# Kernel tuning notes

Hardware: AMD Instinct MI355X
Metric: run time of the kernel (lower is better)

## Reference

```python
import jax, jax.numpy as jnp
import numpy as np

B = 512
DIM_X = 128
DIM_Y = 128
HIDDEN = 512


def setup_inputs() -> dict:
    key = jax.random.key(0)
    kx, ky, kw1, kw2 = jax.random.split(key, 4)
    x = jax.random.normal(kx, (B, DIM_X), dtype=jnp.float32)
    y = jax.random.normal(ky, (B, DIM_Y), dtype=jnp.float32)
    # Glorot-ish scaling for the Dense layers
    W1 = jax.random.normal(kw1, (DIM_X + DIM_Y, HIDDEN), dtype=jnp.float32) * (1.0 / np.sqrt(DIM_X + DIM_Y))
    b1 = jnp.zeros((HIDDEN,), dtype=jnp.float32)
    W2 = jax.random.normal(kw2, (HIDDEN, 1), dtype=jnp.float32) * (1.0 / np.sqrt(HIDDEN))
    b2 = jnp.zeros((1,), dtype=jnp.float32)
    return {"x": x, "y": y, "W1": W1, "b1": b1, "W2": W2, "b2": b2}


def reference(x, y, W1, b1, W2, b2):
    # scores[i, j] = f(concat(x_i, y_j)) with f = Dense(512, relu) -> Dense(1).
    # Since the first Dense is linear in the concatenated input, split W1 into
    # the x-block and y-block and broadcast-sum instead of materializing the
    # [B*B, dim_x+dim_y] concat tensor (same math as tile+concat+matmul).
    dim_x = x.shape[1]
    hx = x @ W1[:dim_x]          # [B, H]
    hy = y @ W1[dim_x:]          # [B, H]
    h = jax.nn.relu(hx[:, None, :] + hy[None, :, :] + b1)  # [B, B, H]
    scores = jnp.einsum('ijh,h->ij', h, W2[:, 0]) + b2[0]   # [B, B]
    return scores
```

## Files before the change

### kernel.cpp

```cpp
#include <hip/hip_runtime.h>


#define BATCH 512
#define DX    128
#define HID   512

typedef _Float16 half2_t __attribute__((ext_vector_type(2)));

static __device__ __forceinline__ half2_t u2h(unsigned int u) {
    union { unsigned int u; half2_t h; } c; c.u = u; return c.h;
}
static __device__ __forceinline__ unsigned int h2u(half2_t h) {
    union { half2_t h; unsigned int u; } c; c.h = h; return c.u;
}

__global__ __launch_bounds__(256) void proj_kernel(
    const float* __restrict__ x, const float* __restrict__ y,
    const float* __restrict__ W1, const float* __restrict__ b1,
    _Float16* __restrict__ hxy)
{
    const int part = blockIdx.y;
    const int row0 = blockIdx.x * 8;
    const int h    = blockIdx.z * 256 + threadIdx.x;
    const float* __restrict__ src = part ? y : x;
    const float* __restrict__ W   = W1 + part * DX * HID;

    __shared__ float s[8][DX];
    {
        const int t = threadIdx.x;
        const int r = t >> 5, c4 = (t & 31) << 2;
        const float4 v = *(const float4*)&src[(row0 + r) * DX + c4];
        s[r][c4] = v.x; s[r][c4 + 1] = v.y; s[r][c4 + 2] = v.z; s[r][c4 + 3] = v.w;
    }
    __syncthreads();

    float acc[8] = {0.f, 0.f, 0.f, 0.f, 0.f, 0.f, 0.f, 0.f};
    #pragma unroll 4
    for (int k = 0; k < DX; ++k) {
        const float w = W[k * HID + h];
        #pragma unroll
        for (int r = 0; r < 8; ++r) acc[r] = fmaf(s[r][k], w, acc[r]);
    }
    const float bias = part ? b1[h] : 0.0f;
    #pragma unroll
    for (int r = 0; r < 8; ++r)
        hxy[(part * BATCH + row0 + r) * HID + h] = (_Float16)(acc[r] + bias);
}

#define TI   128
#define TJ   64
#define HC   64
#define HPW  (HC / 2)
#define ST   33

__global__ __launch_bounds__(512, 2) void score_kernel(
    const _Float16* __restrict__ hxy, const float* __restrict__ W2,
    float* __restrict__ pws)
{
    __shared__ unsigned int sA[TI * ST];
    __shared__ unsigned int sB[TJ * ST];
    __shared__ unsigned int sW[HPW];

    const int i0 = blockIdx.y * TI;
    const int j0 = blockIdx.x * TJ;
    const int hp0 = blockIdx.z * HPW;
    const int tid = threadIdx.x;
    const unsigned int* __restrict__ hx32 = (const unsigned int*)hxy;

    #pragma unroll
    for (int it = 0; it < 2; ++it) {
        const int s = tid + it * 512;
        const int row = s >> 3, q = s & 7;
        const uint4 v = *(const uint4*)&hx32[(i0 + row) * 256 + hp0 + (q << 2)];
        unsigned int* p = &sA[row * ST + (q << 2)];
        p[0] = v.x; p[1] = v.y; p[2] = v.z; p[3] = v.w;
    }
    {
        const int row = tid >> 3, q = tid & 7;
        const uint4 v = *(const uint4*)&hx32[(BATCH + j0 + row) * 256 + hp0 + (q << 2)];
        unsigned int* p = &sB[row * ST + (q << 2)];
        p[0] = v.x; p[1] = v.y; p[2] = v.z; p[3] = v.w;
    }
    if (tid < HPW) {
        const float2 w = *(const float2*)&W2[2 * (hp0 + tid)];
        half2_t wh; wh.x = (_Float16)w.x; wh.y = (_Float16)w.y;
        sW[tid] = h2u(wh);
    }
    __syncthreads();

    const int tx = tid & 15;
    const int ty = tid >> 4;
    const unsigned int* pa = &sA[(ty << 2) * ST];
    const unsigned int* pb = &sB[(tx << 2) * ST];

    float acc[4][4] = {{0.f,0.f,0.f,0.f},{0.f,0.f,0.f,0.f},
                       {0.f,0.f,0.f,0.f},{0.f,0.f,0.f,0.f}};
    const half2_t hz = {(_Float16)0, (_Float16)0};

    #pragma unroll 4
    for (int hp = 0; hp < HPW; ++hp) {
        const half2_t w = u2h(sW[hp]);
        half2_t a[4], b[4];
        #pragma unroll
        for (int r = 0; r < 4; ++r) a[r] = u2h(pa[r * ST + hp]);
        #pragma unroll
        for (int c = 0; c < 4; ++c) b[c] = u2h(pb[c * ST + hp]);
        #pragma unroll
        for (int r = 0; r < 4; ++r)
            #pragma unroll
            for (int c = 0; c < 4; ++c) {
                half2_t t = a[r] + b[c];
                t = __builtin_elementwise_max(t, hz);
                acc[r][c] = __builtin_amdgcn_fdot2(t, w, acc[r][c], false);
            }
    }

    float* dst = pws + blockIdx.z * (BATCH * BATCH);
    const int i = i0 + (ty << 2);
    const int j = j0 + (tx << 2);
    #pragma unroll
    for (int r = 0; r < 4; ++r) {
        float4 v = make_float4(acc[r][0], acc[r][1], acc[r][2], acc[r][3]);
        *(float4*)&dst[(i + r) * BATCH + j] = v;
    }
}

__global__ __launch_bounds__(256) void reduce_kernel(
    const float* __restrict__ pws, const float* __restrict__ b2,
    float* __restrict__ out)
{
    const int idx4 = blockIdx.x * 256 + threadIdx.x;
    const float4* __restrict__ p4 = (const float4*)pws;
    float4 s = p4[idx4];
    #pragma unroll
    for (int z = 1; z < 8; ++z) {
        const float4 v = p4[z * (BATCH * BATCH / 4) + idx4];
        s.x += v.x; s.y += v.y; s.z += v.z; s.w += v.w;
    }
    const float bs = b2[0];
    s.x += bs; s.y += bs; s.z += bs; s.w += bs;
    ((float4*)out)[idx4] = s;
}

extern "C" void kernel_launch(void* const* d_in, const int* in_sizes, int n_in,
                              void* d_out, int out_size, void* d_ws, size_t ws_size,
                              hipStream_t stream) {
    const float* x  = (const float*)d_in[0];
    const float* y  = (const float*)d_in[1];
    const float* W1 = (const float*)d_in[2];
    const float* b1 = (const float*)d_in[3];
    const float* W2 = (const float*)d_in[4];
    const float* b2 = (const float*)d_in[5];
    float* out = (float*)d_out;

    _Float16* hxy = (_Float16*)d_ws;
    float* pws = (float*)((char*)d_ws + (1 << 20));

    proj_kernel<<<dim3(BATCH / 8, 2, 2), 256, 0, stream>>>(x, y, W1, b1, hxy);
    score_kernel<<<dim3(BATCH / TJ, BATCH / TI, HID / HC), 512, 0, stream>>>(hxy, W2, pws);
    reduce_kernel<<<dim3(BATCH * BATCH / 4 / 256), 256, 0, stream>>>(pws, b2, out);
}
```

Before: 88.71 us.

## Fuse projection, score, and reduce into one cooperative kernel with grid syncs

```diff
diff --git a/kernel.cpp b/kernel.cpp
--- a/kernel.cpp
+++ b/kernel.cpp
@@ -1,9 +1,17 @@
 #include <hip/hip_runtime.h>
+#include <hip/hip_cooperative_groups.h>
+
+namespace cg = cooperative_groups;
 
 
 #define BATCH 512
 #define DX    128
 #define HID   512
+
+#define TI   128
+#define TJ   64
+#define HPW  32
+#define ST   33
 
 typedef _Float16 half2_t __attribute__((ext_vector_type(2)));
 
@@ -14,132 +22,134 @@
     union { half2_t h; unsigned int u; } c; c.h = h; return c.u;
 }
 
-__global__ __launch_bounds__(256) void proj_kernel(
+__global__ __launch_bounds__(512, 2) void fused_kernel(
     const float* __restrict__ x, const float* __restrict__ y,
     const float* __restrict__ W1, const float* __restrict__ b1,
-    _Float16* __restrict__ hxy)
+    const float* __restrict__ W2, const float* __restrict__ b2,
+    float* __restrict__ out, _Float16* __restrict__ hxy,
+    unsigned int* __restrict__ pws16)
 {
-    const int part = blockIdx.y;
-    const int row0 = blockIdx.x * 8;
-    const int h    = blockIdx.z * 256 + threadIdx.x;
-    const float* __restrict__ src = part ? y : x;
-    const float* __restrict__ W   = W1 + part * DX * HID;
+    cg::grid_group grid = cg::this_grid();
+    const int b   = blockIdx.x;
+    const int tid = threadIdx.x;
 
-    __shared__ float s[8][DX];
-    {
-        const int t = threadIdx.x;
-        const int r = t >> 5, c4 = (t & 31) << 2;
-        const float4 v = *(const float4*)&src[(row0 + r) * DX + c4];
-        s[r][c4] = v.x; s[r][c4 + 1] = v.y; s[r][c4 + 2] = v.z; s[r][c4 + 3] = v.w;
-    }
-    __syncthreads();
-
-    float acc[8] = {0.f, 0.f, 0.f, 0.f, 0.f, 0.f, 0.f, 0.f};
-    #pragma unroll 4
-    for (int k = 0; k < DX; ++k) {
-        const float w = W[k * HID + h];
-        #pragma unroll
-        for (int r = 0; r < 8; ++r) acc[r] = fmaf(s[r][k], w, acc[r]);
-    }
-    const float bias = part ? b1[h] : 0.0f;
-    #pragma unroll
-    for (int r = 0; r < 8; ++r)
-        hxy[(part * BATCH + row0 + r) * HID + h] = (_Float16)(acc[r] + bias);
-}
-
-#define TI   128
-#define TJ   64
-#define HC   64
-#define HPW  (HC / 2)
-#define ST   33
-
-__global__ __launch_bounds__(512, 2) void score_kernel(
-    const _Float16* __restrict__ hxy, const float* __restrict__ W2,
-    float* __restrict__ pws)
-{
+    __shared__ float        sProj[8][DX];
     __shared__ unsigned int sA[TI * ST];
     __shared__ unsigned int sB[TJ * ST];
     __shared__ unsigned int sW[HPW];
 
-    const int i0 = blockIdx.y * TI;
-    const int j0 = blockIdx.x * TJ;
-    const int hp0 = blockIdx.z * HPW;
-    const int tid = threadIdx.x;
-    const unsigned int* __restrict__ hx32 = (const unsigned int*)hxy;
+    {
+        const int part = b >> 7;
+        const int row0 = ((b & 127) >> 1) * 8;
+        const int h0   = (b & 1) * 256;
+        const float* __restrict__ src = part ? y : x;
+        const float* __restrict__ W   = W1 + part * DX * HID;
 
-    #pragma unroll
-    for (int it = 0; it < 2; ++it) {
-        const int s = tid + it * 512;
-        const int row = s >> 3, q = s & 7;
-        const uint4 v = *(const uint4*)&hx32[(i0 + row) * 256 + hp0 + (q << 2)];
-        unsigned int* p = &sA[row * ST + (q << 2)];
-        p[0] = v.x; p[1] = v.y; p[2] = v.z; p[3] = v.w;
-    }
-    {
-        const int row = tid >> 3, q = tid & 7;
-        const uint4 v = *(const uint4*)&hx32[(BATCH + j0 + row) * 256 + hp0 + (q << 2)];
-        unsigned int* p = &sB[row * ST + (q << 2)];
-        p[0] = v.x; p[1] = v.y; p[2] = v.z; p[3] = v.w;
-    }
-    if (tid < HPW) {
-        const float2 w = *(const float2*)&W2[2 * (hp0 + tid)];
-        half2_t wh; wh.x = (_Float16)w.x; wh.y = (_Float16)w.y;
-        sW[tid] = h2u(wh);
-    }
-    __syncthreads();
+        if (tid < 256) {
+            const int r = tid >> 5, c4 = (tid & 31) << 2;
+            const float4 v = *(const float4*)&src[(row0 + r) * DX + c4];
+            sProj[r][c4]     = v.x; sProj[r][c4 + 1] = v.y;
+            sProj[r][c4 + 2] = v.z; sProj[r][c4 + 3] = v.w;
+        }
+        __syncthreads();
 
-    const int tx = tid & 15;
-    const int ty = tid >> 4;
-    const unsigned int* pa = &sA[(ty << 2) * ST];
-    const unsigned int* pb = &sB[(tx << 2) * ST];
-
-    float acc[4][4] = {{0.f,0.f,0.f,0.f},{0.f,0.f,0.f,0.f},
-                       {0.f,0.f,0.f,0.f},{0.f,0.f,0.f,0.f}};
-    const half2_t hz = {(_Float16)0, (_Float16)0};
-
-    #pragma unroll 4
-    for (int hp = 0; hp < HPW; ++hp) {
-        const half2_t w = u2h(sW[hp]);
-        half2_t a[4], b[4];
-        #pragma unroll
-        for (int r = 0; r < 4; ++r) a[r] = u2h(pa[r * ST + hp]);
-        #pragma unroll
-        for (int c = 0; c < 4; ++c) b[c] = u2h(pb[c * ST + hp]);
+        const int h     = h0 + (tid & 255);
+        const int rbase = (tid >> 8) * 4;
+        float acc[4] = {0.f, 0.f, 0.f, 0.f};
+        #pragma unroll 8
+        for (int k = 0; k < DX; ++k) {
+            const float w = W[k * HID + h];
+            #pragma unroll
+            for (int r = 0; r < 4; ++r) acc[r] = fmaf(sProj[rbase + r][k], w, acc[r]);
+        }
+        const float bias = part ? b1[h] : 0.0f;
         #pragma unroll
         for (int r = 0; r < 4; ++r)
-            #pragma unroll
-            for (int c = 0; c < 4; ++c) {
-                half2_t t = a[r] + b[c];
-                t = __builtin_elementwise_max(t, hz);
-                acc[r][c] = __builtin_amdgcn_fdot2(t, w, acc[r][c], false);
-            }
+            hxy[(part * BATCH + row0 + rbase + r) * HID + h] = (_Float16)(acc[r] + bias);
     }
 
-    float* dst = pws + blockIdx.z * (BATCH * BATCH);
-    const int i = i0 + (ty << 2);
-    const int j = j0 + (tx << 2);
-    #pragma unroll
-    for (int r = 0; r < 4; ++r) {
-        float4 v = make_float4(acc[r][0], acc[r][1], acc[r][2], acc[r][3]);
-        *(float4*)&dst[(i + r) * BATCH + j] = v;
+    grid.sync();
+
+    {
+        const int z   = b & 7;
+        const int j0  = ((b >> 3) & 7) * TJ;
+        const int i0  = (b >> 6) * TI;
+        const int hp0 = z * HPW;
+        const unsigned int* __restrict__ hx32 = (const unsigned int*)hxy;
+
+        #pragma unroll
+        for (int it = 0; it < 2; ++it) {
+            const int s = tid + it * 512;
+            const int row = s >> 3, q = s & 7;
+            const uint4 v = *(const uint4*)&hx32[(i0 + row) * 256 + hp0 + (q << 2)];
+            unsigned int* p = &sA[row * ST + (q << 2)];
+            p[0] = v.x; p[1] = v.y; p[2] = v.z; p[3] = v.w;
+        }
+        {
+            const int row = tid >> 3, q = tid & 7;
+            const uint4 v = *(const uint4*)&hx32[(BATCH + j0 + row) * 256 + hp0 + (q << 2)];
+            unsigned int* p = &sB[row * ST + (q << 2)];
+            p[0] = v.x; p[1] = v.y; p[2] = v.z; p[3] = v.w;
+        }
+        if (tid < HPW) {
+            const float2 w = *(const float2*)&W2[2 * (hp0 + tid)];
+            half2_t wh; wh.x = (_Float16)w.x; wh.y = (_Float16)w.y;
+            sW[tid] = h2u(wh);
+        }
+        __syncthreads();
+
+        const int tx = tid & 15;
+        const int ty = tid >> 4;
+        const unsigned int* pa = &sA[(ty << 2) * ST];
+        const unsigned int* pb = &sB[(tx << 2) * ST];
+
+        float acc[4][4] = {{0.f,0.f,0.f,0.f},{0.f,0.f,0.f,0.f},
+                           {0.f,0.f,0.f,0.f},{0.f,0.f,0.f,0.f}};
+        const half2_t hz = {(_Float16)0, (_Float16)0};
+
+        #pragma unroll 4
+        for (int hp = 0; hp < HPW; ++hp) {
+            const half2_t w = u2h(sW[hp]);
+            half2_t a[4], bb[4];
+            #pragma unroll
+            for (int r = 0; r < 4; ++r) a[r]  = u2h(pa[r * ST + hp]);
+            #pragma unroll
+            for (int c = 0; c < 4; ++c) bb[c] = u2h(pb[c * ST + hp]);
+            #pragma unroll
+            for (int r = 0; r < 4; ++r)
+                #pragma unroll
+                for (int c = 0; c < 4; ++c) {
+                    half2_t t = a[r] + bb[c];
+                    t = __builtin_elementwise_max(t, hz);
+                    acc[r][c] = __builtin_amdgcn_fdot2(t, w, acc[r][c], false);
+                }
+        }
+
+        const int i = i0 + (ty << 2);
+        unsigned int* dst = pws16 + z * (BATCH * BATCH / 2);
+        #pragma unroll
+        for (int r = 0; r < 4; ++r) {
+            half2_t p0, p1;
+            p0.x = (_Float16)acc[r][0]; p0.y = (_Float16)acc[r][1];
+            p1.x = (_Float16)acc[r][2]; p1.y = (_Float16)acc[r][3];
+            uint2 st; st.x = h2u(p0); st.y = h2u(p1);
+            *(uint2*)&dst[(i + r) * (BATCH / 2) + (j0 >> 1) + (tx << 1)] = st;
+        }
     }
-}
 
-__global__ __launch_bounds__(256) void reduce_kernel(
-    const float* __restrict__ pws, const float* __restrict__ b2,
-    float* __restrict__ out)
-{
-    const int idx4 = blockIdx.x * 256 + threadIdx.x;
-    const float4* __restrict__ p4 = (const float4*)pws;
-    float4 s = p4[idx4];
-    #pragma unroll
-    for (int z = 1; z < 8; ++z) {
-        const float4 v = p4[z * (BATCH * BATCH / 4) + idx4];
-        s.x += v.x; s.y += v.y; s.z += v.z; s.w += v.w;
+    grid.sync();
+
+    {
+        const int gid = b * 512 + tid;
+        float s0 = 0.f, s1 = 0.f;
+        #pragma unroll
+        for (int zz = 0; zz < 8; ++zz) {
+            const half2_t v = u2h(pws16[zz * (BATCH * BATCH / 2) + gid]);
+            s0 += (float)v.x; s1 += (float)v.y;
+        }
+        const float bs = b2[0];
+        *(float2*)&out[gid * 2] = make_float2(s0 + bs, s1 + bs);
     }
-    const float bs = b2[0];
-    s.x += bs; s.y += bs; s.z += bs; s.w += bs;
-    ((float4*)out)[idx4] = s;
 }
 
 extern "C" void kernel_launch(void* const* d_in, const int* in_sizes, int n_in,
@@ -153,10 +163,13 @@
     const float* b2 = (const float*)d_in[5];
     float* out = (float*)d_out;
 
-    _Float16* hxy = (_Float16*)d_ws;
-    float* pws = (float*)((char*)d_ws + (1 << 20));
+    _Float16* hxy       = (_Float16*)d_ws;
+    unsigned int* pws16 = (unsigned int*)((char*)d_ws + (1 << 20));
 
-    proj_kernel<<<dim3(BATCH / 8, 2, 2), 256, 0, stream>>>(x, y, W1, b1, hxy);
-    score_kernel<<<dim3(BATCH / TJ, BATCH / TI, HID / HC), 512, 0, stream>>>(hxy, W2, pws);
-    reduce_kernel<<<dim3(BATCH * BATCH / 4 / 256), 256, 0, stream>>>(pws, b2, out);
+    void* args[] = {
+        (void*)&x, (void*)&y, (void*)&W1, (void*)&b1, (void*)&W2, (void*)&b2,
+        (void*)&out, (void*)&hxy, (void*)&pws16
+    };
+    (void)hipLaunchCooperativeKernel((void*)fused_kernel, dim3(256), dim3(512),
+                                     args, 0, stream);
 }
```

After: 152.2 us. 1.72x slower.
